# Kernel tuning notes

Hardware: AMD Instinct MI355X
Metric: run time of the kernel (lower is better)

The kernel has to match this reference:

```python
import jax, jax.numpy as jnp
import numpy as np

B, S, L = 256, 32, 3            # batch of graph pairs, nodes per graph, num GCN layers
FIN, F = 512, 256               # input feature dim, GCN hidden dim
BIG = 99999.0                   # off-diagonal penalty from the module
EG = 128                        # undirected edges per graph


def _make_edges(rng):
    src = rng.integers(0, S, size=(B, EG))
    dst = rng.integers(0, S, size=(B, EG))
    off = (np.arange(B) * S)[:, None]
    s = (src + off).ravel()
    d = (dst + off).ravel()
    ei = np.stack([np.concatenate([s, d]), np.concatenate([d, s])])  # symmetric
    return jnp.asarray(ei, jnp.int32)


def setup_inputs() -> dict:
    key = jax.random.key(0)
    ks = jax.random.split(key, 8)
    rng = np.random.default_rng(0)
    return {
        "x_q": jax.random.normal(ks[0], (B * S, FIN), jnp.float32),
        "x_c": jax.random.normal(ks[1], (B * S, FIN), jnp.float32),
        "W0": jax.random.normal(ks[2], (FIN, F), jnp.float32) * (FIN ** -0.5),
        "b0": jnp.zeros((F,), jnp.float32),
        "W1": jax.random.normal(ks[3], (F, F), jnp.float32) * (F ** -0.5),
        "b1": jnp.zeros((F,), jnp.float32),
        "W2": jax.random.normal(ks[4], (F, F), jnp.float32) * (F ** -0.5),
        "b2": jnp.zeros((F,), jnp.float32),
        "del_p": jax.random.normal(ks[5], (L, F), jnp.float32) * 0.1,
        "ins_p": jax.random.normal(ks[6], (L, F), jnp.float32) * 0.1,
        "ot_w": jax.random.normal(ks[7], (L,), jnp.float32),
        "ot_b": jnp.zeros((1,), jnp.float32),
        "edge_index_q": _make_edges(rng),
        "edge_index_c": _make_edges(rng),
    }


def _gcn(x, ei, W, b):
    # PyG GCNConv: add self-loops, symmetric deg^-1/2 normalization, then linear
    n = x.shape[0]
    loops = jnp.arange(n, dtype=ei.dtype)
    src = jnp.concatenate([ei[0], loops])
    dst = jnp.concatenate([ei[1], loops])
    deg = jax.ops.segment_sum(jnp.ones(src.shape[0], x.dtype), dst, num_segments=n)
    dinv = jax.lax.rsqrt(deg)
    msg = (x @ W)[src] * (dinv[src] * dinv[dst])[:, None]
    return jax.ops.segment_sum(msg, dst, num_segments=n) + b


def _gnn_feats(x, ei, Ws, bs):
    # features stored pre-ReLU (as in GOTSim.GNN); dropout=0 / eval mode
    feats, h = [], x
    for Wl, bl in zip(Ws, bs):
        h = _gcn(h, ei, Wl, bl)
        feats.append(h)
        h = jax.nn.relu(h)
    return feats


def _sim_matrices(x_q, x_c, W0, b0, W1, b1, W2, b2, del_p, ins_p, ei_q, ei_c):
    Ws, bs = (W0, W1, W2), (b0, b1, b2)
    qf = _gnn_feats(x_q, ei_q, Ws, bs)
    cf = _gnn_feats(x_c, ei_c, Ws, bs)
    eye = jnp.eye(S, dtype=x_q.dtype)
    offd = BIG * (1.0 - eye)
    sims = []
    for i in range(L):
        q = qf[i].reshape(B, S, F)
        c = cf[i].reshape(B, S, F)
        main = -jnp.einsum('bqf,bcf->bqc', q, c)                 # [B,S,S]
        dele = (-(q @ del_p[i]))[:, :, None] * eye + offd        # diag_embed + 99999 offdiag
        ins = (-(c @ ins_p[i]))[:, :, None] * eye + offd
        dummy = jnp.zeros((B, S, S), x_q.dtype)
        sims.append(jnp.concatenate([jnp.concatenate([main, dele], 2),
                                     jnp.concatenate([ins, dummy], 2)], 1))
    return jnp.stack(sims, 1)  # [B, L, 2S, 2S]


def _lap(cost):
    # Jonker-Volgenant shortest augmenting path (same optimum as lapjv);
    # returns col4row: column assigned to each row.
    n = cost.shape[0]
    u = np.zeros(n)
    v = np.zeros(n)
    col4row = np.full(n, -1, np.int64)
    row4col = np.full(n, -1, np.int64)
    for cur in range(n):
        shortest = np.full(n, np.inf)
        path = np.full(n, -1, np.int64)
        SC = np.zeros(n, bool)
        sr_rows = [cur]
        i, min_val, sink = cur, 0.0, -1
        while sink == -1:
            r = min_val + cost[i] - u[i] - v
            upd = (~SC) & (r < shortest)
            shortest[upd] = r[upd]
            path[upd] = i
            masked = np.where(SC, np.inf, shortest)
            j = int(np.argmin(masked))
            min_val = masked[j]
            SC[j] = True
            if row4col[j] < 0:
                sink = j
            else:
                i = int(row4col[j])
                sr_rows.append(i)
        u[cur] += min_val
        for i2 in sr_rows[1:]:
            u[i2] += min_val - shortest[col4row[i2]]
        v[SC] -= min_val - shortest[SC]
        j = sink
        while True:
            i2 = int(path[j])
            row4col[j] = i2
            col4row[i2], j = j, int(col4row[i2])
            if i2 == cur:
                break
    return col4row


def _plans(sim_np):
    # plan[b,l] = eye[col4row] as in dense_wasserstein_distance_v3
    n = sim_np.shape[-1]
    eye = np.eye(n, dtype=np.float32)
    flat = sim_np.reshape(-1, n, n)
    out = np.empty_like(flat, dtype=np.float32)
    for k in range(flat.shape[0]):
        out[k] = eye[_lap(flat[k].astype(np.float64))]
    return out.reshape(sim_np.shape)


def reference(x_q, x_c, W0, b0, W1, b1, W2, b2, del_p, ins_p, ot_w, ot_b,
              edge_index_q, edge_index_c):
    sim = _sim_matrices(x_q, x_c, W0, b0, W1, b1, W2, b2, del_p, ins_p,
                        edge_index_q, edge_index_c)
    plans = jnp.asarray(_plans(np.asarray(sim)))
    mcost = jnp.sum(sim * plans, axis=(2, 3))          # [B, L]
    mcost_norm = 2.0 * mcost / (2.0 * S)               # qsize + csize = 2S
    scores = mcost_norm @ ot_w + ot_b[0]               # Linear(L, 1)
    return jax.nn.sigmoid(scores)                      # is_sig=True -> [B]
```

## Files before the change

### kernel.cpp

```cpp
#include <hip/hip_runtime.h>
#include <math.h>


#define LAP_INF 1e30f

typedef __attribute__((ext_vector_type(8))) short short8;
typedef __attribute__((ext_vector_type(4))) float f32x4;

__device__ __forceinline__ unsigned short bf16_rne(float x) {
  unsigned u = __float_as_uint(x);
  return (unsigned short)((u + 0x7fffu + ((u >> 16) & 1u)) >> 16);
}
__device__ __forceinline__ void split2(float x, unsigned short& h, unsigned short& l) {
  h = bf16_rne(x);
  l = (unsigned short)(__float_as_uint(x - __uint_as_float((unsigned)h << 16)) >> 16);
}

__global__ __launch_bounds__(512) void prep_k(const int* __restrict__ eiq,
                                              const int* __restrict__ eic,
                                              const float* __restrict__ W0,
                                              const float* __restrict__ W1,
                                              const float* __restrict__ W2,
                                              float* __restrict__ adj,
                                              unsigned short* __restrict__ WP,
                                              int ne) {
  const int bx = blockIdx.x;
  const int t = threadIdx.x;
  if (bx < 512) {
    __shared__ float A[1024];
    __shared__ float dinv[32];
    const int g = bx & 255, side = bx >> 8;
    const int* ei = side ? eic : eiq;
    const int half = ne >> 1;
    for (int k = t; k < 1024; k += 512) A[k] = 0.f;
    __syncthreads();
    if (t < 256) {
      int e = (t < 128) ? (g * 128 + t) : (half + g * 128 + (t - 128));
      int s = ei[e];
      int d = ei[ne + e];
      if ((d >> 5) == g)
        atomicAdd(&A[(d & 31) * 32 + (s & 31)], 1.0f);
    }
    __syncthreads();
    if (t < 32) A[t * 32 + t] += 1.0f;
    __syncthreads();
    if (t < 32) {
      float dsum = 0.f;
#pragma unroll
      for (int j = 0; j < 32; ++j) dsum += A[t * 32 + j];
      dinv[t] = rsqrtf(dsum);
    }
    __syncthreads();
    float* dstA = adj + (size_t)(side * 256 + g) * 1024;
    for (int k = t; k < 1024; k += 512)
      dstA[k] = A[k] * dinv[k >> 5] * dinv[k & 31];
  } else {
    __shared__ float tile[32][33];
    int r = bx - 512;
    int z, x, y;
    if (r < 128)      { z = 0; x = r & 15; y = r >> 4; }
    else if (r < 192) { z = 1; r -= 128; x = r & 7; y = r >> 3; }
    else              { z = 2; r -= 192; x = r & 7; y = r >> 3; }
    const float* W = (z == 0) ? W0 : (z == 1) ? W1 : W2;
    const int K = (z == 0) ? 512 : 256;
    unsigned short* WH = WP + ((z == 0) ? 0 : (z == 1) ? 262144 : 393216);
    unsigned short* WL = WH + ((z == 0) ? 131072 : 65536);
    const int k0 = x * 32, n0 = y * 32;
    const int tr = t & 31, tc = t >> 5;
    for (int rr = tc; rr < 32; rr += 16)
      tile[rr][tr] = W[(size_t)(k0 + rr) * 256 + n0 + tr];
    __syncthreads();
    for (int rr = tc; rr < 32; rr += 16) {
      float v = tile[tr][rr];
      unsigned short h, l;
      split2(v, h, l);
      WH[(size_t)(n0 + rr) * K + k0 + tr] = h;
      WL[(size_t)(n0 + rr) * K + k0 + tr] = l;
    }
  }
}

template <int CTRL>
__device__ __forceinline__ float dpp_ror_min(float x) {
  int y = __builtin_amdgcn_update_dpp(0, __float_as_int(x), CTRL, 0xf, 0xf, true);
  return fminf(x, __int_as_float(y));
}
template <int CTRL>
__device__ __forceinline__ float dpp_ror_add(float x) {
  int y = __builtin_amdgcn_update_dpp(0, __float_as_int(x), CTRL, 0xf, 0xf, true);
  return x + __int_as_float(y);
}
__device__ __forceinline__ float rdlane_f(float x, int l) {
  return __int_as_float(__builtin_amdgcn_readlane(__float_as_int(x), l));
}
__device__ __forceinline__ float wave_min32(float x) {
  x = dpp_ror_min<0x121>(x);
  x = dpp_ror_min<0x122>(x);
  x = dpp_ror_min<0x124>(x);
  x = dpp_ror_min<0x128>(x);
  return fminf(rdlane_f(x, 0), rdlane_f(x, 16));
}
#define LDS_FENCE() __asm__ volatile("s_waitcnt lgkmcnt(0)" ::: "memory")

__global__ __launch_bounds__(512) void gnn_k(
    const float* __restrict__ xq, const float* __restrict__ xc,
    const unsigned short* __restrict__ WH0, const unsigned short* __restrict__ WL0,
    const unsigned short* __restrict__ WH1, const unsigned short* __restrict__ WL1,
    const unsigned short* __restrict__ WH2, const unsigned short* __restrict__ WL2,
    const float* __restrict__ adj,
    const float* __restrict__ b0, const float* __restrict__ b1,
    const float* __restrict__ b2,
    const float* __restrict__ delp, const float* __restrict__ insp,
    const float* __restrict__ ot_w, const float* __restrict__ ot_b,
    float* __restrict__ out) {
  __shared__ __align__(16) unsigned short Pp[2][64 * 264];
  __shared__ float Ys[64][258];
  __shared__ float adjs[2048];
  __shared__ __align__(16) float simsbuf[3][1024];
  __shared__ float dq[32], dic[32];
  __shared__ float vlbuf[3][32];
  __shared__ float mc[4];
  unsigned short* As0 = (unsigned short*)&simsbuf[0][0];
  unsigned short* As1 = As0 + 64 * 40;

  const int b = blockIdx.x, t = threadIdx.x;
  const int wave = t >> 6, lane = t & 63;
  const int lrow = lane & 15, kgrp = lane >> 4;

  for (int k = t; k < 2048; k += 512)
    adjs[k] = adj[(size_t)((k >> 10) * 256 + b) * 1024 + (k & 1023)];

  for (int l = 0; l < 3; ++l) {
    const unsigned short* WH = (l == 0) ? WH0 : (l == 1) ? WH1 : WH2;
    const unsigned short* WL = (l == 0) ? WL0 : (l == 1) ? WL1 : WL2;
    const float* bias = (l == 0) ? b0 : (l == 1) ? b1 : b2;

    f32x4 acc[4][2];
#pragma unroll
    for (int i = 0; i < 4; ++i)
#pragma unroll
      for (int j = 0; j < 2; ++j) acc[i][j] = (f32x4){0.f, 0.f, 0.f, 0.f};

    if (l == 0) {
      const int arow = t >> 3, aseg = t & 7;
      const float* Asrc = (arow < 32)
          ? (xq + (size_t)(b * 32 + arow) * 512)
          : (xc + (size_t)(b * 32 + (arow - 32)) * 512);
      for (int kt = 0; kt < 512; kt += 32) {
        {
          float4 xv = *(const float4*)(Asrc + kt + aseg * 4);
          ushort4 h, lo;
          split2(xv.x, h.x, lo.x); split2(xv.y, h.y, lo.y);
          split2(xv.z, h.z, lo.z); split2(xv.w, h.w, lo.w);
          *(ushort4*)&As0[arow * 40 + aseg * 4] = h;
          *(ushort4*)&As1[arow * 40 + aseg * 4] = lo;
        }
        __syncthreads();
        short8 ah[4], al[4];
#pragma unroll
        for (int mf = 0; mf < 4; ++mf) {
          const int off = (mf * 16 + lrow) * 40 + kgrp * 8;
          ah[mf] = *(const short8*)&As0[off];
          al[mf] = *(const short8*)&As1[off];
        }
#pragma unroll
        for (int nf = 0; nf < 2; ++nf) {
          const int row = wave * 32 + nf * 16 + lrow;
          short8 bh = *(const short8*)&WH[(size_t)row * 512 + kt + kgrp * 8];
          short8 bl = *(const short8*)&WL[(size_t)row * 512 + kt + kgrp * 8];
#pragma unroll
          for (int mf = 0; mf < 4; ++mf) {
            acc[mf][nf] = __builtin_amdgcn_mfma_f32_16x16x32_bf16(ah[mf], bh, acc[mf][nf], 0, 0, 0);
            acc[mf][nf] = __builtin_amdgcn_mfma_f32_16x16x32_bf16(ah[mf], bl, acc[mf][nf], 0, 0, 0);
            acc[mf][nf] = __builtin_amdgcn_mfma_f32_16x16x32_bf16(al[mf], bh, acc[mf][nf], 0, 0, 0);
          }
        }
        __syncthreads();
      }
    } else {
#pragma unroll
      for (int kt8 = 0; kt8 < 8; ++kt8) {
        const int kt = kt8 * 32;
        short8 ah[4], al[4];
#pragma unroll
        for (int mf = 0; mf < 4; ++mf) {
          const int off = (mf * 16 + lrow) * 264 + kt + kgrp * 8;
          ah[mf] = *(const short8*)&Pp[0][off];
          al[mf] = *(const short8*)&Pp[1][off];
        }
#pragma unroll
        for (int nf = 0; nf < 2; ++nf) {
          const int row = wave * 32 + nf * 16 + lrow;
          short8 bh = *(const short8*)&WH[(size_t)row * 256 + kt + kgrp * 8];
          short8 bl = *(const short8*)&WL[(size_t)row * 256 + kt + kgrp * 8];
#pragma unroll
          for (int mf = 0; mf < 4; ++mf) {
            acc[mf][nf] = __builtin_amdgcn_mfma_f32_16x16x32_bf16(ah[mf], bh, acc[mf][nf], 0, 0, 0);
            acc[mf][nf] = __builtin_amdgcn_mfma_f32_16x16x32_bf16(ah[mf], bl, acc[mf][nf], 0, 0, 0);
            acc[mf][nf] = __builtin_amdgcn_mfma_f32_16x16x32_bf16(al[mf], bh, acc[mf][nf], 0, 0, 0);
          }
        }
      }
    }
#pragma unroll
    for (int mf = 0; mf < 4; ++mf)
#pragma unroll
      for (int nf = 0; nf < 2; ++nf)
#pragma unroll
        for (int r = 0; r < 4; ++r)
          Ys[mf * 16 + kgrp * 4 + r][wave * 32 + nf * 16 + lrow] = acc[mf][nf][r];
    __syncthreads();

    const int side = t >> 8, f = t & 255;
    float pv[32];
    {
      const float* A = adjs + side * 1024;
      float y[32];
#pragma unroll
      for (int j = 0; j < 32; ++j) y[j] = Ys[side * 32 + j][f];
      const float bf = bias[f];
#pragma unroll 4
      for (int i = 0; i < 32; ++i) {
        float a = bf;
#pragma unroll
        for (int j = 0; j < 32; ++j) a = fmaf(A[i * 32 + j], y[j], a);
        pv[i] = a;
      }
#pragma unroll
      for (int i = 0; i < 32; ++i) {
        Ys[side * 32 + i][f] = pv[i];
        unsigned short h, lo;
        split2(pv[i], h, lo);
        Pp[0][(side * 32 + i) * 264 + f] = h;
        Pp[1][(side * 32 + i) * 264 + f] = lo;
      }
    }
    __syncthreads();
    {
      const int row = t >> 3, sub = t & 7;
      const float* pvec = ((row < 32) ? delp : insp) + l * 256;
      const float* X = &Ys[row][0];
      float a = 0.f;
#pragma unroll 8
      for (int k = 0; k < 32; ++k) {
        int idx = sub * 32 + ((k + row) & 31);
        a = fmaf(X[idx], pvec[idx], a);
      }
      a += __shfl_xor(a, 1);
      a += __shfl_xor(a, 2);
      a += __shfl_xor(a, 4);
      if ((t & 7) == 0) { if (row < 32) dq[row] = -a; else dic[row & 31] = -a; }
    }
    __syncthreads();
    if (wave < 4) {
      const int mf = wave >> 1, nf = wave & 1;
      f32x4 sa = (f32x4){0.f, 0.f, 0.f, 0.f};
#pragma unroll
      for (int kt8 = 0; kt8 < 8; ++kt8) {
        const int kt = kt8 * 32;
        const int aoff = (mf * 16 + lrow) * 264 + kt + kgrp * 8;
        const int boff = (32 + nf * 16 + lrow) * 264 + kt + kgrp * 8;
        short8 ah = *(const short8*)&Pp[0][aoff];
        short8 al = *(const short8*)&Pp[1][aoff];
        short8 bh = *(const short8*)&Pp[0][boff];
        short8 bl = *(const short8*)&Pp[1][boff];
        sa = __builtin_amdgcn_mfma_f32_16x16x32_bf16(ah, bh, sa, 0, 0, 0);
        sa = __builtin_amdgcn_mfma_f32_16x16x32_bf16(ah, bl, sa, 0, 0, 0);
        sa = __builtin_amdgcn_mfma_f32_16x16x32_bf16(al, bh, sa, 0, 0, 0);
      }
#pragma unroll
      for (int r = 0; r < 4; ++r) {
        const int m = mf * 16 + kgrp * 4 + r;
        const int n = nf * 16 + lrow;
        simsbuf[l][m * 32 + n] = fminf(-sa[r], dq[m] + dic[n]);
      }
    }
    __syncthreads();
    if (l < 2) {
#pragma unroll
      for (int i = 0; i < 32; ++i) {
        unsigned short h, lo;
        split2(fmaxf(pv[i], 0.f), h, lo);
        Pp[0][(side * 32 + i) * 264 + f] = h;
        Pp[1][(side * 32 + i) * 264 + f] = lo;
      }
      __syncthreads();
    }
  }

  if (wave < 3) {
    if (lane < 32) {
      float* Cl = &simsbuf[wave][0];
      float* vl = &vlbuf[wave][0];
      float minv = LAP_INF;
      int imin = 0;
#pragma unroll
      for (int i = 0; i < 32; ++i) {
        float val = Cl[i * 32 + lane];
        if (val < minv) { minv = val; imin = i; }
      }
      float vj = minv;
      float u = 0.0f;
      int col4row = -1;
      int row4col = -1;
#pragma unroll
      for (int r = 0; r < 32; ++r) {
        unsigned long long bal = __ballot(imin == r);
        if (bal) {
          int j = 63 - __clzll(bal);
          if (lane == j) row4col = r;
          if (lane == r) col4row = j;
        }
      }
      unsigned long long freemask = __ballot(col4row < 0);

      vl[lane] = vj;
      LDS_FENCE();
      {
        float min1 = LAP_INF, min2 = LAP_INF;
        int j1 = -1;
#pragma unroll
        for (int j = 0; j < 32; ++j) {
          float s = Cl[lane * 32 + j] - vl[j];
          if (s < min1) { min2 = min1; min1 = s; j1 = j; }
          else if (s < min2) { min2 = s; }
        }
        float delta = 0.f;
        if (col4row >= 0) {
          delta = (j1 == col4row) ? min2 : min1;
          u = delta;
        }
        int sidx = (row4col < 0) ? lane : row4col;
        float dv = __shfl(delta, sidx);
        if (row4col >= 0) vj -= dv;
      }

      if (freemask) {
        vl[lane] = vj;
        LDS_FENCE();
        float rs = LAP_INF;
#pragma unroll
        for (int j = 0; j < 32; ++j) rs = fminf(rs, Cl[lane * 32 + j] - vl[j]);
        if (col4row < 0) u = rs;
        unsigned long long fm = freemask;
        while (fm) {
          const int r = __ffsll(fm) - 1;
          fm &= fm - 1;
          float m = rdlane_f(rs, r);
          float s = Cl[r * 32 + lane] - vj;
          unsigned long long bal = __ballot((s == m) && (row4col < 0));
          if (bal) {
            int j = __ffsll(bal) - 1;
            if (lane == j) row4col = r;
            if (lane == r) col4row = j;
          }
        }
        freemask = __ballot(col4row < 0);
      }

      while (freemask) {
        const int cur = __ffsll(freemask) - 1;
        freemask &= freemask - 1;
        float shortest = LAP_INF;
        int path = -1;
        bool SC = false;
        int i = cur;
        float minval = 0.0f;
        int sink;
        while (true) {
          float ui = rdlane_f(u, i);
          float r = minval + Cl[i * 32 + lane] - ui - vj;
          bool better = (!SC) && (r < shortest);
          shortest = better ? r : shortest;
          path = better ? i : path;
          float masked = SC ? LAP_INF : shortest;
          float mv = wave_min32(masked);
          unsigned long long bal = __ballot(masked == mv);
          int j = __ffsll(bal) - 1;
          minval = mv;
          SC = SC || (lane == j);
          int rj = __builtin_amdgcn_readlane(row4col, j);
          if (rj < 0) { sink = j; break; }
          i = rj;
        }
        unsigned long long scmask = __ballot(SC);
        if (SC) vj -= minval - shortest;
        int sidx = (col4row < 0) ? lane : col4row;
        float sh_j0 = __shfl(shortest, sidx);
        bool scanned = (col4row >= 0) && ((scmask >> col4row) & 1ull) && (col4row != sink);
        if (lane == cur) u += minval;
        else if (scanned) u += minval - sh_j0;
        int j = sink;
        while (true) {
          int i2 = __builtin_amdgcn_readlane(path, j);
          int jn = __builtin_amdgcn_readlane(col4row, i2);
          if (lane == j) row4col = i2;
          if (lane == i2) col4row = j;
          j = jn;
          if (i2 == cur) break;
        }
      }
      float cc = Cl[lane * 32 + col4row];
      cc = dpp_ror_add<0x121>(cc);
      cc = dpp_ror_add<0x122>(cc);
      cc = dpp_ror_add<0x124>(cc);
      cc = dpp_ror_add<0x128>(cc);
      float tot = rdlane_f(cc, 0) + rdlane_f(cc, 16);
      if (lane == 0) mc[wave] = tot;
    }
  }
  __syncthreads();
  if (t == 0) {
    float s = ot_b[0];
#pragma unroll
    for (int l2 = 0; l2 < 3; ++l2)
      s += mc[l2] * (1.0f / 32.0f) * ot_w[l2];
    out[b] = 1.0f / (1.0f + expf(-s));
  }
}

extern "C" void kernel_launch(void* const* d_in, const int* in_sizes, int n_in,
                              void* d_out, int out_size, void* d_ws, size_t ws_size,
                              hipStream_t stream) {
  const float* x_q  = (const float*)d_in[0];
  const float* x_c  = (const float*)d_in[1];
  const float* W0   = (const float*)d_in[2];
  const float* b0   = (const float*)d_in[3];
  const float* W1   = (const float*)d_in[4];
  const float* b1   = (const float*)d_in[5];
  const float* W2   = (const float*)d_in[6];
  const float* b2   = (const float*)d_in[7];
  const float* delp = (const float*)d_in[8];
  const float* insp = (const float*)d_in[9];
  const float* ot_w = (const float*)d_in[10];
  const float* ot_b = (const float*)d_in[11];
  const int* ei_q   = (const int*)d_in[12];
  const int* ei_c   = (const int*)d_in[13];
  float* out = (float*)d_out;

  float* ws  = (float*)d_ws;
  float* adj = ws;
  unsigned short* WP = (unsigned short*)(adj + 524288);
  unsigned short* WH0 = WP;
  unsigned short* WL0 = WP + 131072;
  unsigned short* WH1 = WP + 262144;
  unsigned short* WL1 = WP + 327680;
  unsigned short* WH2 = WP + 393216;
  unsigned short* WL2 = WP + 458752;

  const int ne = in_sizes[12] / 2;

  prep_k<<<768, 512, 0, stream>>>(ei_q, ei_c, W0, W1, W2, adj, WP, ne);
  gnn_k<<<256, 512, 0, stream>>>(x_q, x_c, WH0, WL0, WH1, WL1, WH2, WL2,
                                 adj, b0, b1, b2, delp, insp, ot_w, ot_b, out);
}
```

Before: 177.8 us.

## Double-buffer layer-0 A tiles and prefetch weights in GNN kernel

```diff
diff --git a/kernel.cpp b/kernel.cpp
--- a/kernel.cpp
+++ b/kernel.cpp
@@ -102,7 +102,7 @@
 }
 #define LDS_FENCE() __asm__ volatile("s_waitcnt lgkmcnt(0)" ::: "memory")
 
-__global__ __launch_bounds__(512) void gnn_k(
+__global__ __launch_bounds__(512, 2) void gnn_k(
     const float* __restrict__ xq, const float* __restrict__ xc,
     const unsigned short* __restrict__ WH0, const unsigned short* __restrict__ WL0,
     const unsigned short* __restrict__ WH1, const unsigned short* __restrict__ WL1,
@@ -120,8 +120,8 @@
   __shared__ float dq[32], dic[32];
   __shared__ float vlbuf[3][32];
   __shared__ float mc[4];
-  unsigned short* As0 = (unsigned short*)&simsbuf[0][0];
-  unsigned short* As1 = As0 + 64 * 40;
+  unsigned short* SA0 = &Pp[0][0];
+  unsigned short* SA1 = &Pp[1][0];
 
   const int b = blockIdx.x, t = threadIdx.x;
   const int wave = t >> 6, lane = t & 63;
@@ -146,35 +146,61 @@
       const float* Asrc = (arow < 32)
           ? (xq + (size_t)(b * 32 + arow) * 512)
           : (xc + (size_t)(b * 32 + (arow - 32)) * 512);
+      float4 xv = *(const float4*)(Asrc + aseg * 4);
+      short8 pbh[2], pbl[2];
+#pragma unroll
+      for (int nf = 0; nf < 2; ++nf) {
+        const int row = wave * 32 + nf * 16 + lrow;
+        pbh[nf] = *(const short8*)&WH[(size_t)row * 512 + kgrp * 8];
+        pbl[nf] = *(const short8*)&WL[(size_t)row * 512 + kgrp * 8];
+      }
+      {
+        ushort4 h, lo;
+        split2(xv.x, h.x, lo.x); split2(xv.y, h.y, lo.y);
+        split2(xv.z, h.z, lo.z); split2(xv.w, h.w, lo.w);
+        *(ushort4*)&SA0[arow * 40 + aseg * 4] = h;
+        *(ushort4*)&SA1[arow * 40 + aseg * 4] = lo;
+      }
+      __syncthreads();
+      int buf = 0;
       for (int kt = 0; kt < 512; kt += 32) {
-        {
-          float4 xv = *(const float4*)(Asrc + kt + aseg * 4);
+        const bool more = (kt + 32 < 512);
+        float4 xn;
+        if (more) xn = *(const float4*)(Asrc + kt + 32 + aseg * 4);
+        short8 bh0 = pbh[0], bh1 = pbh[1];
+        short8 bl0 = pbl[0], bl1 = pbl[1];
+        if (more) {
+#pragma unroll
+          for (int nf = 0; nf < 2; ++nf) {
+            const int row = wave * 32 + nf * 16 + lrow;
+            pbh[nf] = *(const short8*)&WH[(size_t)row * 512 + kt + 32 + kgrp * 8];
+            pbl[nf] = *(const short8*)&WL[(size_t)row * 512 + kt + 32 + kgrp * 8];
+          }
+        }
+        short8 ah[4], al[4];
+#pragma unroll
+        for (int mf = 0; mf < 4; ++mf) {
+          const int off = buf * 2560 + (mf * 16 + lrow) * 40 + kgrp * 8;
+          ah[mf] = *(const short8*)&SA0[off];
+          al[mf] = *(const short8*)&SA1[off];
+        }
+#pragma unroll
+        for (int mf = 0; mf < 4; ++mf) {
+          acc[mf][0] = __builtin_amdgcn_mfma_f32_16x16x32_bf16(ah[mf], bh0, acc[mf][0], 0, 0, 0);
+          acc[mf][0] = __builtin_amdgcn_mfma_f32_16x16x32_bf16(ah[mf], bl0, acc[mf][0], 0, 0, 0);
+          acc[mf][0] = __builtin_amdgcn_mfma_f32_16x16x32_bf16(al[mf], bh0, acc[mf][0], 0, 0, 0);
+          acc[mf][1] = __builtin_amdgcn_mfma_f32_16x16x32_bf16(ah[mf], bh1, acc[mf][1], 0, 0, 0);
+          acc[mf][1] = __builtin_amdgcn_mfma_f32_16x16x32_bf16(ah[mf], bl1, acc[mf][1], 0, 0, 0);
+          acc[mf][1] = __builtin_amdgcn_mfma_f32_16x16x32_bf16(al[mf], bh1, acc[mf][1], 0, 0, 0);
+        }
+        if (more) {
           ushort4 h, lo;
-          split2(xv.x, h.x, lo.x); split2(xv.y, h.y, lo.y);
-          split2(xv.z, h.z, lo.z); split2(xv.w, h.w, lo.w);
-          *(ushort4*)&As0[arow * 40 + aseg * 4] = h;
-          *(ushort4*)&As1[arow * 40 + aseg * 4] = lo;
-        }
-        __syncthreads();
-        short8 ah[4], al[4];
-#pragma unroll
-        for (int mf = 0; mf < 4; ++mf) {
-          const int off = (mf * 16 + lrow) * 40 + kgrp * 8;
-          ah[mf] = *(const short8*)&As0[off];
-          al[mf] = *(const short8*)&As1[off];
-        }
-#pragma unroll
-        for (int nf = 0; nf < 2; ++nf) {
-          const int row = wave * 32 + nf * 16 + lrow;
-          short8 bh = *(const short8*)&WH[(size_t)row * 512 + kt + kgrp * 8];
-          short8 bl = *(const short8*)&WL[(size_t)row * 512 + kt + kgrp * 8];
-#pragma unroll
-          for (int mf = 0; mf < 4; ++mf) {
-            acc[mf][nf] = __builtin_amdgcn_mfma_f32_16x16x32_bf16(ah[mf], bh, acc[mf][nf], 0, 0, 0);
-            acc[mf][nf] = __builtin_amdgcn_mfma_f32_16x16x32_bf16(ah[mf], bl, acc[mf][nf], 0, 0, 0);
-            acc[mf][nf] = __builtin_amdgcn_mfma_f32_16x16x32_bf16(al[mf], bh, acc[mf][nf], 0, 0, 0);
-          }
-        }
+          split2(xn.x, h.x, lo.x); split2(xn.y, h.y, lo.y);
+          split2(xn.z, h.z, lo.z); split2(xn.w, h.w, lo.w);
+          *(ushort4*)&SA0[(buf ^ 1) * 2560 + arow * 40 + aseg * 4] = h;
+          *(ushort4*)&SA1[(buf ^ 1) * 2560 + arow * 40 + aseg * 4] = lo;
+        }
+        buf ^= 1;
         __syncthreads();
       }
     } else {
@@ -243,7 +269,7 @@
       float a = 0.f;
 #pragma unroll 8
       for (int k = 0; k < 32; ++k) {
-        int idx = sub * 32 + ((k + row) & 31);
+        int idx = sub + 8 * k;
         a = fmaf(X[idx], pvec[idx], a);
       }
       a += __shfl_xor(a, 1);
```

Measured after the change: 169.7 us. -4.5%, faster.
